# Kernel optimization log

Measured on AMD Instinct MI355X. Metric: run time of the kernel, lower is better.

The kernel has to match this reference:

```python
import jax, jax.numpy as jnp
import numpy as np
from jax import lax

LENGTH = 9
PAD = LENGTH // 2          # 4
WIN_SIZE = LENGTH * LENGTH # 81
EPS = 1e-09
ALPHA = 0.01
PENALTY = 'l2'


def setup_inputs() -> dict:
    key = jax.random.key(0)
    k1, k2, k3 = jax.random.split(key, 3)
    B, C, H, W = 8, 1, 1024, 1024
    I = jax.random.normal(k1, (B, C, H, W), dtype=jnp.float32)
    J = jax.random.normal(k2, (B, C, H, W), dtype=jnp.float32)
    s = jax.random.normal(k3, (B, 2, H, W), dtype=jnp.float32)
    # buffer: all-ones box filter, shape [out=1, in=C, k, k]
    sum_filt = jnp.ones((1, C, LENGTH, LENGTH), dtype=jnp.float32)
    return {"I": I, "J": J, "s": s, "sum_filt": sum_filt}


def _box_conv(x, filt):
    # NCHW conv with 'same' padding (odd kernel), stride 1 -> [B,1,H,W]
    return lax.conv_general_dilated(
        x, filt, window_strides=(1, 1),
        padding=[(PAD, PAD), (PAD, PAD)],
        dimension_numbers=('NCHW', 'OIHW', 'NCHW'))


def _compute_local_sums(I, J, filt):
    I2, J2, IJ = I * I, J * J, I * J
    I_sum = _box_conv(I, filt)
    J_sum = _box_conv(J, filt)
    I2_sum = _box_conv(I2, filt)
    J2_sum = _box_conv(J2, filt)
    IJ_sum = _box_conv(IJ, filt)
    u_I = I_sum / WIN_SIZE
    u_J = J_sum / WIN_SIZE
    cross = IJ_sum - u_J * I_sum - u_I * J_sum + u_I * u_J * WIN_SIZE
    I_var = I2_sum - 2 * u_I * I_sum + u_I * u_I * WIN_SIZE
    J_var = J2_sum - 2 * u_J * J_sum + u_J * u_J * WIN_SIZE
    return I_var, J_var, cross


def _gradient_loss(s):
    dy = jnp.abs(s[:, :, 1:, :] - s[:, :, :-1, :])
    dx = jnp.abs(s[:, :, :, 1:] - s[:, :, :, :-1])
    if PENALTY == 'l2':
        dy = dy * dy
        dx = dx * dx
    return (jnp.mean(dx) + jnp.mean(dy)) / 2.0


def reference(I, J, s, sum_filt):
    I_var, J_var, cross = _compute_local_sums(I, J, sum_filt)
    cc = cross * cross / (I_var * J_var + EPS)
    ncc_loss = -jnp.mean(cc)
    smoothness_loss = _gradient_loss(s) * ALPHA
    total_loss = ncc_loss + smoothness_loss
    return (total_loss, ncc_loss, smoothness_loss)
```

## Files before the change

kernel.cpp:

```cpp
#include <hip/hip_runtime.h>

#define HH 1024
#define WW 1024
#define NB 8
#define TY 16
#define NSTRIPS (HH / TY)
#define NCC_BLOCKS (NB * NSTRIPS)
#define SROWS 16
#define NROWS_S (NB * 2 * HH)
#define SM_BLOCKS (NROWS_S / SROWS)


__device__ __forceinline__ void load_win(const float* __restrict__ row, int q, float w[12]) {
    const float4* r4 = (const float4*)row;
    float4 m = (q > 0) ? r4[q - 1] : float4{0.f, 0.f, 0.f, 0.f};
    float4 c = r4[q];
    float4 p = (q < WW / 4 - 1) ? r4[q + 1] : float4{0.f, 0.f, 0.f, 0.f};
    w[0] = m.x; w[1] = m.y; w[2] = m.z; w[3] = m.w;
    w[4] = c.x; w[5] = c.y; w[6] = c.z; w[7] = c.w;
    w[8] = p.x; w[9] = p.y; w[10] = p.z; w[11] = p.w;
}

template <bool ADD>
__device__ __forceinline__ void accum_row(const float* __restrict__ Ib, const float* __restrict__ Jb,
                                          int y, int q,
                                          float vsI[4], float vsJ[4],
                                          float vsI2[4], float vsJ2[4], float vsIJ[4]) {
    if (y < 0 || y >= HH) return;
    float wI[12], wJ[12];
    load_win(Ib + (size_t)y * WW, q, wI);
    load_win(Jb + (size_t)y * WW, q, wJ);
    float a2[12], b2[12], ab[12];
#pragma unroll
    for (int k = 0; k < 12; ++k) {
        a2[k] = wI[k] * wI[k];
        b2[k] = wJ[k] * wJ[k];
        ab[k] = wI[k] * wJ[k];
    }
    float sI = 0.f, sJ = 0.f, s2I = 0.f, s2J = 0.f, sIJ = 0.f;
#pragma unroll
    for (int k = 0; k < 9; ++k) { sI += wI[k]; sJ += wJ[k]; s2I += a2[k]; s2J += b2[k]; sIJ += ab[k]; }
#pragma unroll
    for (int c = 0; c < 4; ++c) {
        if (c > 0) {
            sI  += wI[c + 8] - wI[c - 1];
            sJ  += wJ[c + 8] - wJ[c - 1];
            s2I += a2[c + 8] - a2[c - 1];
            s2J += b2[c + 8] - b2[c - 1];
            sIJ += ab[c + 8] - ab[c - 1];
        }
        if (ADD) { vsI[c] += sI; vsJ[c] += sJ; vsI2[c] += s2I; vsJ2[c] += s2J; vsIJ[c] += sIJ; }
        else     { vsI[c] -= sI; vsJ[c] -= sJ; vsI2[c] -= s2I; vsJ2[c] -= s2J; vsIJ[c] -= sIJ; }
    }
}


__global__ __launch_bounds__(256) void fused_kernel(const float* __restrict__ I,
                                                    const float* __restrict__ J,
                                                    const float* __restrict__ S,
                                                    float* __restrict__ ws) {
    __shared__ float red[8];
    const int bid = blockIdx.x;
    const int t = threadIdx.x;
    const int lane = t & 63;
    const int wid = t >> 6;

    if (bid < NCC_BLOCKS) {
        const int b = bid >> 6;
        const int strip = bid & 63;
        const int y0 = strip * TY;
        const int q = t;
        const float* Ib = I + (size_t)b * HH * WW;
        const float* Jb = J + (size_t)b * HH * WW;

        float vsI[4] = {0.f, 0.f, 0.f, 0.f};
        float vsJ[4] = {0.f, 0.f, 0.f, 0.f};
        float vsI2[4] = {0.f, 0.f, 0.f, 0.f};
        float vsJ2[4] = {0.f, 0.f, 0.f, 0.f};
        float vsIJ[4] = {0.f, 0.f, 0.f, 0.f};
        float ccacc = 0.f;

#pragma unroll 2
        for (int k = 0; k < 8; ++k)
            accum_row<true>(Ib, Jb, y0 - 4 + k, q, vsI, vsJ, vsI2, vsJ2, vsIJ);

        constexpr float RW = 1.0f / 81.0f;
#pragma unroll 2
        for (int k = 0; k < TY; ++k) {
            const int y = y0 + k;
            accum_row<true>(Ib, Jb, y + 4, q, vsI, vsJ, vsI2, vsJ2, vsIJ);
#pragma unroll
            for (int c = 0; c < 4; ++c) {
                const float Is = vsI[c], Js = vsJ[c];
                const float uI = Is * RW, uJ = Js * RW;
                const float cross = vsIJ[c] - uJ * Is - uI * Js + uI * uJ * 81.0f;
                const float Iv = vsI2[c] - 2.0f * uI * Is + uI * uI * 81.0f;
                const float Jv = vsJ2[c] - 2.0f * uJ * Js + uJ * uJ * 81.0f;
                ccacc += cross * cross / (Iv * Jv + 1e-9f);
            }
            accum_row<false>(Ib, Jb, y - 4, q, vsI, vsJ, vsI2, vsJ2, vsIJ);
        }

#pragma unroll
        for (int o = 32; o; o >>= 1) ccacc += __shfl_down(ccacc, o);
        if (lane == 0) red[wid] = ccacc;
        __syncthreads();
        if (t == 0) ws[bid] = red[0] + red[1] + red[2] + red[3];
    } else {
        const int sb = bid - NCC_BLOCKS;
        const int r0 = sb * SROWS;
        const float* base = S + (size_t)r0 * WW;
        float dxacc = 0.f, dyacc = 0.f;

        float4 v = ((const float4*)base)[t];
#pragma unroll 2
        for (int k = 0; k < SROWS; ++k) {
            const int y = (r0 + k) & (HH - 1);
            const float* rp = base + (size_t)k * WW;
            float d0 = v.y - v.x, d1 = v.z - v.y, d2 = v.w - v.z;
            dxacc += d0 * d0 + d1 * d1 + d2 * d2;
            if (t < 255) { const float vr = rp[4 * t + 4]; const float d3 = vr - v.w; dxacc += d3 * d3; }
            if (y < HH - 1) {
                const float4 vn = ((const float4*)(rp + WW))[t];
                const float e0 = vn.x - v.x, e1 = vn.y - v.y, e2 = vn.z - v.z, e3 = vn.w - v.w;
                dyacc += e0 * e0 + e1 * e1 + e2 * e2 + e3 * e3;
                v = vn;
            }
        }

#pragma unroll
        for (int o = 32; o; o >>= 1) {
            dxacc += __shfl_down(dxacc, o);
            dyacc += __shfl_down(dyacc, o);
        }
        if (lane == 0) { red[wid] = dxacc; red[4 + wid] = dyacc; }
        __syncthreads();
        if (t == 0) {
            ws[NCC_BLOCKS + sb] = red[0] + red[1] + red[2] + red[3];
            ws[NCC_BLOCKS + SM_BLOCKS + sb] = red[4] + red[5] + red[6] + red[7];
        }
    }
}


__global__ __launch_bounds__(256) void finalize_kernel(const float* __restrict__ ws,
                                                       float* __restrict__ out) {
    __shared__ double sd[256];
    __shared__ double res[3];
    const int t = threadIdx.x;
    double cc = 0.0, dx = 0.0, dy = 0.0;
    for (int i = t; i < NCC_BLOCKS; i += 256) cc += (double)ws[i];
    for (int i = t; i < SM_BLOCKS; i += 256) dx += (double)ws[NCC_BLOCKS + i];
    for (int i = t; i < SM_BLOCKS; i += 256) dy += (double)ws[NCC_BLOCKS + SM_BLOCKS + i];

    sd[t] = cc; __syncthreads();
    for (int s = 128; s; s >>= 1) { if (t < s) sd[t] += sd[t + s]; __syncthreads(); }
    if (t == 0) res[0] = sd[0];
    __syncthreads();
    sd[t] = dx; __syncthreads();
    for (int s = 128; s; s >>= 1) { if (t < s) sd[t] += sd[t + s]; __syncthreads(); }
    if (t == 0) res[1] = sd[0];
    __syncthreads();
    sd[t] = dy; __syncthreads();
    for (int s = 128; s; s >>= 1) { if (t < s) sd[t] += sd[t + s]; __syncthreads(); }
    if (t == 0) {
        res[2] = sd[0];
        const double ncc = -(res[0] / ((double)NB * 1.0 * HH * WW));
        const double mdx = res[1] / ((double)NB * 2.0 * HH * (WW - 1));
        const double mdy = res[2] / ((double)NB * 2.0 * (HH - 1) * WW);
        const double smooth = 0.01 * 0.5 * (mdx + mdy);
        out[0] = (float)(ncc + smooth);
        out[1] = (float)ncc;
        out[2] = (float)smooth;
    }
}

extern "C" void kernel_launch(void* const* d_in, const int* in_sizes, int n_in,
                              void* d_out, int out_size, void* d_ws, size_t ws_size,
                              hipStream_t stream) {
    const float* I = (const float*)d_in[0];
    const float* J = (const float*)d_in[1];
    const float* S = (const float*)d_in[2];
    float* ws = (float*)d_ws;
    float* out = (float*)d_out;

    fused_kernel<<<NCC_BLOCKS + SM_BLOCKS, 256, 0, stream>>>(I, J, S, ws);
    finalize_kernel<<<1, 256, 0, stream>>>(ws, out);
}
```

Before: 174.5 us.

## Separate box filter into vertical column sums plus shared-memory horizontal slide

Each thread now keeps running vertical column sums for its own four pixels and reads only one float4 per row of I and J, where before it loaded three float4s and built horizontal sums every row. The horizontal 9-wide sums come from neighbours' column sums exchanged through shared memory, which costs two block barriers per output row. The strip height drops from 16 to 8 so there are more blocks, and NCC and smoothness blocks are interleaved by block-index parity. The variance and cross formulas are simplified algebraically and the division is replaced by a fast hardware reciprocal, which is slightly less accurate.

```diff
diff --git a/kernel.cpp b/kernel.cpp
--- a/kernel.cpp
+++ b/kernel.cpp
@@ -3,111 +3,119 @@
 #define HH 1024
 #define WW 1024
 #define NB 8
-#define TY 16
-#define NSTRIPS (HH / TY)
-#define NCC_BLOCKS (NB * NSTRIPS)
+#define TY 8
+#define NCC_BLOCKS (NB * (HH / TY))
 #define SROWS 16
-#define NROWS_S (NB * 2 * HH)
-#define SM_BLOCKS (NROWS_S / SROWS)
+#define SM_BLOCKS (NB * 2 * HH / SROWS)
+#define RW (1.0f / 81.0f)
 
-
-__device__ __forceinline__ void load_win(const float* __restrict__ row, int q, float w[12]) {
-    const float4* r4 = (const float4*)row;
-    float4 m = (q > 0) ? r4[q - 1] : float4{0.f, 0.f, 0.f, 0.f};
-    float4 c = r4[q];
-    float4 p = (q < WW / 4 - 1) ? r4[q + 1] : float4{0.f, 0.f, 0.f, 0.f};
-    w[0] = m.x; w[1] = m.y; w[2] = m.z; w[3] = m.w;
-    w[4] = c.x; w[5] = c.y; w[6] = c.z; w[7] = c.w;
-    w[8] = p.x; w[9] = p.y; w[10] = p.z; w[11] = p.w;
-}
-
-template <bool ADD>
-__device__ __forceinline__ void accum_row(const float* __restrict__ Ib, const float* __restrict__ Jb,
-                                          int y, int q,
-                                          float vsI[4], float vsJ[4],
-                                          float vsI2[4], float vsJ2[4], float vsIJ[4]) {
+template <int SGN>
+__device__ __forceinline__ void vrow(const float* __restrict__ Ib, const float* __restrict__ Jb,
+                                     int y, int t,
+                                     float vI[4], float vJ[4],
+                                     float vI2[4], float vJ2[4], float vIJ[4]) {
     if (y < 0 || y >= HH) return;
-    float wI[12], wJ[12];
-    load_win(Ib + (size_t)y * WW, q, wI);
-    load_win(Jb + (size_t)y * WW, q, wJ);
-    float a2[12], b2[12], ab[12];
-#pragma unroll
-    for (int k = 0; k < 12; ++k) {
-        a2[k] = wI[k] * wI[k];
-        b2[k] = wJ[k] * wJ[k];
-        ab[k] = wI[k] * wJ[k];
-    }
-    float sI = 0.f, sJ = 0.f, s2I = 0.f, s2J = 0.f, sIJ = 0.f;
-#pragma unroll
-    for (int k = 0; k < 9; ++k) { sI += wI[k]; sJ += wJ[k]; s2I += a2[k]; s2J += b2[k]; sIJ += ab[k]; }
+    const float4 i4 = ((const float4*)(Ib + (size_t)y * WW))[t];
+    const float4 j4 = ((const float4*)(Jb + (size_t)y * WW))[t];
+    const float fi[4] = {i4.x, i4.y, i4.z, i4.w};
+    const float fj[4] = {j4.x, j4.y, j4.z, j4.w};
 #pragma unroll
     for (int c = 0; c < 4; ++c) {
-        if (c > 0) {
-            sI  += wI[c + 8] - wI[c - 1];
-            sJ  += wJ[c + 8] - wJ[c - 1];
-            s2I += a2[c + 8] - a2[c - 1];
-            s2J += b2[c + 8] - b2[c - 1];
-            sIJ += ab[c + 8] - ab[c - 1];
+        const float a = fi[c], b = fj[c];
+        if (SGN > 0) {
+            vI[c] += a; vJ[c] += b;
+            vI2[c] = fmaf(a, a, vI2[c]);
+            vJ2[c] = fmaf(b, b, vJ2[c]);
+            vIJ[c] = fmaf(a, b, vIJ[c]);
+        } else {
+            vI[c] -= a; vJ[c] -= b;
+            vI2[c] = fmaf(-a, a, vI2[c]);
+            vJ2[c] = fmaf(-b, b, vJ2[c]);
+            vIJ[c] = fmaf(-a, b, vIJ[c]);
         }
-        if (ADD) { vsI[c] += sI; vsJ[c] += sJ; vsI2[c] += s2I; vsJ2[c] += s2J; vsIJ[c] += sIJ; }
-        else     { vsI[c] -= sI; vsJ[c] -= sJ; vsI2[c] -= s2I; vsJ2[c] -= s2J; vsIJ[c] -= sIJ; }
     }
 }
 
+__device__ __forceinline__ void hslide(const float4 l, const float4 r, const float own[4], float hs[4]) {
+    float h = l.x + l.y + l.z + l.w + own[0] + own[1] + own[2] + own[3] + r.x;
+    hs[0] = h;
+    h += r.y - l.x; hs[1] = h;
+    h += r.z - l.y; hs[2] = h;
+    h += r.w - l.z; hs[3] = h;
+}
 
 __global__ __launch_bounds__(256) void fused_kernel(const float* __restrict__ I,
                                                     const float* __restrict__ J,
                                                     const float* __restrict__ S,
                                                     float* __restrict__ ws) {
+    __shared__ float4 cs[5][258];
     __shared__ float red[8];
     const int bid = blockIdx.x;
     const int t = threadIdx.x;
     const int lane = t & 63;
     const int wid = t >> 6;
 
-    if (bid < NCC_BLOCKS) {
-        const int b = bid >> 6;
-        const int strip = bid & 63;
+    if ((bid & 1) == 0) {
+        const int nb = bid >> 1;
+        const int b = nb >> 7;
+        const int strip = nb & 127;
         const int y0 = strip * TY;
-        const int q = t;
         const float* Ib = I + (size_t)b * HH * WW;
         const float* Jb = J + (size_t)b * HH * WW;
 
-        float vsI[4] = {0.f, 0.f, 0.f, 0.f};
-        float vsJ[4] = {0.f, 0.f, 0.f, 0.f};
-        float vsI2[4] = {0.f, 0.f, 0.f, 0.f};
-        float vsJ2[4] = {0.f, 0.f, 0.f, 0.f};
-        float vsIJ[4] = {0.f, 0.f, 0.f, 0.f};
+        float vI[4] = {0, 0, 0, 0}, vJ[4] = {0, 0, 0, 0};
+        float vI2[4] = {0, 0, 0, 0}, vJ2[4] = {0, 0, 0, 0}, vIJ[4] = {0, 0, 0, 0};
         float ccacc = 0.f;
 
-#pragma unroll 2
+        if (t < 5) {
+            cs[t][0] = float4{0, 0, 0, 0};
+            cs[t][257] = float4{0, 0, 0, 0};
+        }
+
+#pragma unroll
         for (int k = 0; k < 8; ++k)
-            accum_row<true>(Ib, Jb, y0 - 4 + k, q, vsI, vsJ, vsI2, vsJ2, vsIJ);
+            vrow<1>(Ib, Jb, y0 - 4 + k, t, vI, vJ, vI2, vJ2, vIJ);
 
-        constexpr float RW = 1.0f / 81.0f;
 #pragma unroll 2
         for (int k = 0; k < TY; ++k) {
             const int y = y0 + k;
-            accum_row<true>(Ib, Jb, y + 4, q, vsI, vsJ, vsI2, vsJ2, vsIJ);
+            vrow<1>(Ib, Jb, y + 4, t, vI, vJ, vI2, vJ2, vIJ);
+
+            cs[0][t + 1] = float4{vI[0], vI[1], vI[2], vI[3]};
+            cs[1][t + 1] = float4{vJ[0], vJ[1], vJ[2], vJ[3]};
+            cs[2][t + 1] = float4{vI2[0], vI2[1], vI2[2], vI2[3]};
+            cs[3][t + 1] = float4{vJ2[0], vJ2[1], vJ2[2], vJ2[3]};
+            cs[4][t + 1] = float4{vIJ[0], vIJ[1], vIJ[2], vIJ[3]};
+            __syncthreads();
+
+            float hsI[4], hsJ[4], hsI2[4], hsJ2[4], hsIJ[4];
+            hslide(cs[0][t], cs[0][t + 2], vI, hsI);
+            hslide(cs[1][t], cs[1][t + 2], vJ, hsJ);
+            hslide(cs[2][t], cs[2][t + 2], vI2, hsI2);
+            hslide(cs[3][t], cs[3][t + 2], vJ2, hsJ2);
+            hslide(cs[4][t], cs[4][t + 2], vIJ, hsIJ);
+            __syncthreads();
+
 #pragma unroll
             for (int c = 0; c < 4; ++c) {
-                const float Is = vsI[c], Js = vsJ[c];
-                const float uI = Is * RW, uJ = Js * RW;
-                const float cross = vsIJ[c] - uJ * Is - uI * Js + uI * uJ * 81.0f;
-                const float Iv = vsI2[c] - 2.0f * uI * Is + uI * uI * 81.0f;
-                const float Jv = vsJ2[c] - 2.0f * uJ * Js + uJ * uJ * 81.0f;
-                ccacc += cross * cross / (Iv * Jv + 1e-9f);
+                const float Is = hsI[c], Js = hsJ[c];
+                const float cross = fmaf(-Is * Js, RW, hsIJ[c]);
+                const float Iv = fmaf(-Is * Is, RW, hsI2[c]);
+                const float Jv = fmaf(-Js * Js, RW, hsJ2[c]);
+                const float den = fmaf(Iv, Jv, 1e-9f);
+                ccacc += cross * cross * __builtin_amdgcn_rcpf(den);
             }
-            accum_row<false>(Ib, Jb, y - 4, q, vsI, vsJ, vsI2, vsJ2, vsIJ);
+
+            vrow<-1>(Ib, Jb, y - 4, t, vI, vJ, vI2, vJ2, vIJ);
         }
 
 #pragma unroll
         for (int o = 32; o; o >>= 1) ccacc += __shfl_down(ccacc, o);
         if (lane == 0) red[wid] = ccacc;
         __syncthreads();
-        if (t == 0) ws[bid] = red[0] + red[1] + red[2] + red[3];
+        if (t == 0) ws[nb] = red[0] + red[1] + red[2] + red[3];
     } else {
-        const int sb = bid - NCC_BLOCKS;
+        const int sb = bid >> 1;
         const int r0 = sb * SROWS;
         const float* base = S + (size_t)r0 * WW;
         float dxacc = 0.f, dyacc = 0.f;
@@ -117,7 +125,7 @@
         for (int k = 0; k < SROWS; ++k) {
             const int y = (r0 + k) & (HH - 1);
             const float* rp = base + (size_t)k * WW;
-            float d0 = v.y - v.x, d1 = v.z - v.y, d2 = v.w - v.z;
+            const float d0 = v.y - v.x, d1 = v.z - v.y, d2 = v.w - v.z;
             dxacc += d0 * d0 + d1 * d1 + d2 * d2;
             if (t < 255) { const float vr = rp[4 * t + 4]; const float d3 = vr - v.w; dxacc += d3 * d3; }
             if (y < HH - 1) {
@@ -141,7 +149,6 @@
         }
     }
 }
-
 
 __global__ __launch_bounds__(256) void finalize_kernel(const float* __restrict__ ws,
                                                        float* __restrict__ out) {
```

After: 182.5 us. +4.6%, slower.
